# Kernel tuning notes

Hardware: AMD Instinct MI355X
Metric: run time of the kernel (lower is better)

## Reference

```python
import jax, jax.numpy as jnp
import numpy as np
from jax import lax

GAMMA = 0.99
LAM = 0.95


def setup_inputs() -> dict:
    key = jax.random.key(0)
    k1, k2, k3 = jax.random.split(key, 3)
    B, S = 4096, 4096
    rewards = jax.random.normal(k1, (B, S), dtype=jnp.float32)
    values = jax.random.normal(k2, (B, S), dtype=jnp.float32)
    next_values = jax.random.normal(k3, (B,), dtype=jnp.float32)
    return {"rewards": rewards, "values": values, "next_values": next_values}


def reference(rewards, values, next_values):
    # delta_t = r_t + gamma * V(s_{t+1}) - V(s_t); bootstrap with next_values at t = S-1
    next_v_full = jnp.concatenate([values[:, 1:], next_values[:, None]], axis=1)  # [B,S]
    deltas = rewards + GAMMA * next_v_full - values  # [B,S]

    # Reverse-time recurrence: A_t = delta_t + gamma*lam * A_{t+1}
    def step(adv, delta_t):
        adv = delta_t + (GAMMA * LAM) * adv
        return adv, adv

    deltas_rev = jnp.swapaxes(deltas, 0, 1)[::-1]  # [S,B], time-reversed
    init = jnp.zeros(rewards.shape[0], dtype=rewards.dtype)
    _, advs_rev = lax.scan(step, init, deltas_rev)  # [S,B]
    advantages = jnp.swapaxes(advs_rev[::-1], 0, 1)  # [B,S]

    returns = advantages + values
    # original detaches both outputs
    return (lax.stop_gradient(advantages), lax.stop_gradient(returns))
```

## Files before the change

kernel.cpp:

```cpp
#include <hip/hip_runtime.h>


#define GAMMA 0.99f
#define LAM   0.95f

typedef float fvec4 __attribute__((ext_vector_type(4)));

constexpr int S_LEN = 4096;
constexpr int TPB   = 256;
constexpr int NSEG  = 4;

__global__ __launch_bounds__(TPB) void gae_kernel(const float* __restrict__ rewards,
                                                  const float* __restrict__ values,
                                                  const float* __restrict__ next_values,
                                                  float* __restrict__ out, int B) {
    __shared__ float Tlds[16];

    const int b    = blockIdx.x;
    const int tid  = threadIdx.x;
    const int lane = tid & 63;
    const int w    = tid >> 6;
    const float c  = GAMMA * LAM;
    const float q4 = c * c * c * c;

    const float* vrow = values  + (size_t)b * S_LEN;
    const float* rrow = rewards + (size_t)b * S_LEN;
    const float  nv   = next_values[b];

    fvec4 v4[NSEG], r4[NSEG];
    float vn[NSEG];
#pragma unroll
    for (int s = 0; s < NSEG; ++s) {
        const int g0 = s * 1024 + 4 * tid;
        v4[s] = *(const fvec4*)(vrow + g0);
        r4[s] = *(const fvec4*)(rrow + g0);
    }
#pragma unroll
    for (int s = 0; s < NSEG; ++s) {
        const int g4 = s * 1024 + 4 * tid + 4;
        if (s == NSEG - 1 && tid == TPB - 1) vn[s] = nv;
        else                                 vn[s] = vrow[g4];
    }

    float a0[NSEG], a1[NSEG], a2[NSEG], a3[NSEG];
    float Wn[NSEG];
    float Tk = 0.f;
    float qs[6];
    {
        float qd = q4;
#pragma unroll
        for (int k = 0; k < 6; ++k) { qs[k] = qd; qd *= qd; }
    }
    const float Q256 = qs[5] * qs[5];

#pragma unroll
    for (int s = 0; s < NSEG; ++s) {
        float d3 = fmaf(GAMMA, vn[s],    r4[s].w) - v4[s].w;
        float d2 = fmaf(GAMMA, v4[s].w,  r4[s].z) - v4[s].z;
        float d1 = fmaf(GAMMA, v4[s].z,  r4[s].y) - v4[s].y;
        float d0 = fmaf(GAMMA, v4[s].y,  r4[s].x) - v4[s].x;
        float t3 = d3;
        float t2 = fmaf(c, t3, d2);
        float t1 = fmaf(c, t2, d1);
        float t0 = fmaf(c, t1, d0);
        a3[s] = t3; a2[s] = t2; a1[s] = t1; a0[s] = t0;

        float x = t0;
#pragma unroll
        for (int dlog = 0; dlog < 6; ++dlog) {
            int d = 1 << dlog;
            float other = __shfl_down(x, d);
            if (lane + d < 64) x = fmaf(qs[dlog], other, x);
        }
        Wn[s] = __shfl_down(x, 1);
        float tb = __shfl(x, 0);
        if (lane == s) Tk = tb;
    }

    if (lane < NSEG) Tlds[lane * 4 + w] = Tk;
    __syncthreads();
    float tv = (lane < 16) ? Tlds[lane] : 0.f;
    {
        float Qd = Q256;
#pragma unroll
        for (int dlog = 0; dlog < 4; ++dlog) {
            int d = 1 << dlog;
            float other = __shfl_down(tv, d);
            if (lane + d < 16) tv = fmaf(Qd, other, tv);
            Qd *= Qd;
        }
    }

    float qp = 1.f;
    {
        int e = 63 - lane;
#pragma unroll
        for (int k = 0; k < 6; ++k) if ((e >> k) & 1) qp *= qs[k];
    }

    float* adv_row = out + (size_t)b * S_LEN;
    float* ret_row = out + (size_t)B * S_LEN + (size_t)b * S_LEN;
    const float c2 = c * c, c3 = c2 * c;
#pragma unroll
    for (int s = 0; s < NSEG; ++s) {
        const int m = s * 4 + w;
        float Cm = (m == 15) ? 0.f : __shfl(tv, m + 1);
        float ct = (lane == 63) ? Cm : fmaf(qp, Cm, Wn[s]);
        float o3 = fmaf(c,  ct, a3[s]);
        float o2 = fmaf(c2, ct, a2[s]);
        float o1 = fmaf(c3, ct, a1[s]);
        float o0 = fmaf(q4, ct, a0[s]);
        const int g0 = s * 1024 + 4 * tid;
        fvec4 av; av.x = o0; av.y = o1; av.z = o2; av.w = o3;
        fvec4 rv = av + v4[s];
        __builtin_nontemporal_store(av, (fvec4*)(adv_row + g0));
        __builtin_nontemporal_store(rv, (fvec4*)(ret_row + g0));
    }
}

extern "C" void kernel_launch(void* const* d_in, const int* in_sizes, int n_in,
                              void* d_out, int out_size, void* d_ws, size_t ws_size,
                              hipStream_t stream) {
    const float* rewards     = (const float*)d_in[0];
    const float* values      = (const float*)d_in[1];
    const float* next_values = (const float*)d_in[2];
    float* out = (float*)d_out;
    const int B = in_sizes[2];
    gae_kernel<<<B, TPB, 0, stream>>>(rewards, values, next_values, out, B);
}
```

Measured before the change: 44.01 us.

## Process four rows per block with double-buffered register prefetch

Each block now handles four rows instead of one. The next row's values and rewards are loaded into a second register set while the current row is being scanned, and the LDS slot for the cross-wave carries alternates between rows. The intent is to hide global load latency behind the shuffle scan and to cut block launch overhead. In exchange the grid shrinks to B/4 blocks and register pressure roughly doubles, which can lower occupancy on a memory-bound kernel. The launch also assumes B is divisible by four.

```diff
diff --git a/kernel.cpp b/kernel.cpp
--- a/kernel.cpp
+++ b/kernel.cpp
@@ -9,42 +9,20 @@
 constexpr int S_LEN = 4096;
 constexpr int TPB   = 256;
 constexpr int NSEG  = 4;
+constexpr int ROWS  = 4;
 
 __global__ __launch_bounds__(TPB) void gae_kernel(const float* __restrict__ rewards,
                                                   const float* __restrict__ values,
                                                   const float* __restrict__ next_values,
                                                   float* __restrict__ out, int B) {
-    __shared__ float Tlds[16];
+    __shared__ float Tlds[2][16];
 
-    const int b    = blockIdx.x;
     const int tid  = threadIdx.x;
     const int lane = tid & 63;
     const int w    = tid >> 6;
     const float c  = GAMMA * LAM;
     const float q4 = c * c * c * c;
 
-    const float* vrow = values  + (size_t)b * S_LEN;
-    const float* rrow = rewards + (size_t)b * S_LEN;
-    const float  nv   = next_values[b];
-
-    fvec4 v4[NSEG], r4[NSEG];
-    float vn[NSEG];
-#pragma unroll
-    for (int s = 0; s < NSEG; ++s) {
-        const int g0 = s * 1024 + 4 * tid;
-        v4[s] = *(const fvec4*)(vrow + g0);
-        r4[s] = *(const fvec4*)(rrow + g0);
-    }
-#pragma unroll
-    for (int s = 0; s < NSEG; ++s) {
-        const int g4 = s * 1024 + 4 * tid + 4;
-        if (s == NSEG - 1 && tid == TPB - 1) vn[s] = nv;
-        else                                 vn[s] = vrow[g4];
-    }
-
-    float a0[NSEG], a1[NSEG], a2[NSEG], a3[NSEG];
-    float Wn[NSEG];
-    float Tk = 0.f;
     float qs[6];
     {
         float qd = q4;
@@ -52,70 +30,105 @@
         for (int k = 0; k < 6; ++k) { qs[k] = qd; qd *= qd; }
     }
     const float Q256 = qs[5] * qs[5];
-
-#pragma unroll
-    for (int s = 0; s < NSEG; ++s) {
-        float d3 = fmaf(GAMMA, vn[s],    r4[s].w) - v4[s].w;
-        float d2 = fmaf(GAMMA, v4[s].w,  r4[s].z) - v4[s].z;
-        float d1 = fmaf(GAMMA, v4[s].z,  r4[s].y) - v4[s].y;
-        float d0 = fmaf(GAMMA, v4[s].y,  r4[s].x) - v4[s].x;
-        float t3 = d3;
-        float t2 = fmaf(c, t3, d2);
-        float t1 = fmaf(c, t2, d1);
-        float t0 = fmaf(c, t1, d0);
-        a3[s] = t3; a2[s] = t2; a1[s] = t1; a0[s] = t0;
-
-        float x = t0;
-#pragma unroll
-        for (int dlog = 0; dlog < 6; ++dlog) {
-            int d = 1 << dlog;
-            float other = __shfl_down(x, d);
-            if (lane + d < 64) x = fmaf(qs[dlog], other, x);
-        }
-        Wn[s] = __shfl_down(x, 1);
-        float tb = __shfl(x, 0);
-        if (lane == s) Tk = tb;
-    }
-
-    if (lane < NSEG) Tlds[lane * 4 + w] = Tk;
-    __syncthreads();
-    float tv = (lane < 16) ? Tlds[lane] : 0.f;
-    {
-        float Qd = Q256;
-#pragma unroll
-        for (int dlog = 0; dlog < 4; ++dlog) {
-            int d = 1 << dlog;
-            float other = __shfl_down(tv, d);
-            if (lane + d < 16) tv = fmaf(Qd, other, tv);
-            Qd *= Qd;
-        }
-    }
-
     float qp = 1.f;
     {
         int e = 63 - lane;
 #pragma unroll
         for (int k = 0; k < 6; ++k) if ((e >> k) & 1) qp *= qs[k];
     }
+    const float c2 = c * c, c3 = c2 * c;
 
-    float* adv_row = out + (size_t)b * S_LEN;
-    float* ret_row = out + (size_t)B * S_LEN + (size_t)b * S_LEN;
-    const float c2 = c * c, c3 = c2 * c;
+    const int b0 = blockIdx.x * ROWS;
+
+    auto LOAD = [&](int b, fvec4 (&v4)[NSEG], fvec4 (&r4)[NSEG], float (&vn)[NSEG]) {
+        const float* vrow = values  + (size_t)b * S_LEN;
+        const float* rrow = rewards + (size_t)b * S_LEN;
 #pragma unroll
-    for (int s = 0; s < NSEG; ++s) {
-        const int m = s * 4 + w;
-        float Cm = (m == 15) ? 0.f : __shfl(tv, m + 1);
-        float ct = (lane == 63) ? Cm : fmaf(qp, Cm, Wn[s]);
-        float o3 = fmaf(c,  ct, a3[s]);
-        float o2 = fmaf(c2, ct, a2[s]);
-        float o1 = fmaf(c3, ct, a1[s]);
-        float o0 = fmaf(q4, ct, a0[s]);
-        const int g0 = s * 1024 + 4 * tid;
-        fvec4 av; av.x = o0; av.y = o1; av.z = o2; av.w = o3;
-        fvec4 rv = av + v4[s];
-        __builtin_nontemporal_store(av, (fvec4*)(adv_row + g0));
-        __builtin_nontemporal_store(rv, (fvec4*)(ret_row + g0));
-    }
+        for (int s = 0; s < NSEG; ++s) {
+            const int g0 = s * 1024 + 4 * tid;
+            v4[s] = *(const fvec4*)(vrow + g0);
+            r4[s] = *(const fvec4*)(rrow + g0);
+        }
+#pragma unroll
+        for (int s = 0; s < NSEG; ++s) {
+            const int g4 = s * 1024 + 4 * tid + 4;
+            if (s == NSEG - 1 && tid == TPB - 1) vn[s] = next_values[b];
+            else                                 vn[s] = vrow[g4];
+        }
+    };
+
+    auto COMPUTE = [&](int b, int par, fvec4 (&v4)[NSEG], fvec4 (&r4)[NSEG],
+                       float (&vn)[NSEG]) {
+        float a0[NSEG], a1[NSEG], a2[NSEG], a3[NSEG], Wn[NSEG];
+        float Tk = 0.f;
+#pragma unroll
+        for (int s = 0; s < NSEG; ++s) {
+            float d3 = fmaf(GAMMA, vn[s],   r4[s].w) - v4[s].w;
+            float d2 = fmaf(GAMMA, v4[s].w, r4[s].z) - v4[s].z;
+            float d1 = fmaf(GAMMA, v4[s].z, r4[s].y) - v4[s].y;
+            float d0 = fmaf(GAMMA, v4[s].y, r4[s].x) - v4[s].x;
+            float t3 = d3;
+            float t2 = fmaf(c, t3, d2);
+            float t1 = fmaf(c, t2, d1);
+            float t0 = fmaf(c, t1, d0);
+            a3[s] = t3; a2[s] = t2; a1[s] = t1; a0[s] = t0;
+
+            float x = t0;
+#pragma unroll
+            for (int dlog = 0; dlog < 6; ++dlog) {
+                int d = 1 << dlog;
+                float other = __shfl_down(x, d);
+                if (lane + d < 64) x = fmaf(qs[dlog], other, x);
+            }
+            Wn[s] = __shfl_down(x, 1);
+            float tb = __shfl(x, 0);
+            if (lane == s) Tk = tb;
+        }
+
+        if (lane < NSEG) Tlds[par][lane * 4 + w] = Tk;
+        __syncthreads();
+        float tv = (lane < 16) ? Tlds[par][lane] : 0.f;
+        {
+            float Qd = Q256;
+#pragma unroll
+            for (int dlog = 0; dlog < 4; ++dlog) {
+                int d = 1 << dlog;
+                float other = __shfl_down(tv, d);
+                if (lane + d < 16) tv = fmaf(Qd, other, tv);
+                Qd *= Qd;
+            }
+        }
+
+        float* adv_row = out + (size_t)b * S_LEN;
+        float* ret_row = out + (size_t)B * S_LEN + (size_t)b * S_LEN;
+#pragma unroll
+        for (int s = 0; s < NSEG; ++s) {
+            const int m = s * 4 + w;
+            float Cm = (m == 15) ? 0.f : __shfl(tv, m + 1);
+            float ct = (lane == 63) ? Cm : fmaf(qp, Cm, Wn[s]);
+            float o3 = fmaf(c,  ct, a3[s]);
+            float o2 = fmaf(c2, ct, a2[s]);
+            float o1 = fmaf(c3, ct, a1[s]);
+            float o0 = fmaf(q4, ct, a0[s]);
+            const int g0 = s * 1024 + 4 * tid;
+            fvec4 av; av.x = o0; av.y = o1; av.z = o2; av.w = o3;
+            fvec4 rv = av + v4[s];
+            __builtin_nontemporal_store(av, (fvec4*)(adv_row + g0));
+            __builtin_nontemporal_store(rv, (fvec4*)(ret_row + g0));
+        }
+    };
+
+    fvec4 vA[NSEG], rA[NSEG], vB[NSEG], rB[NSEG];
+    float vnA[NSEG], vnB[NSEG];
+
+    LOAD(b0 + 0, vA, rA, vnA);
+    LOAD(b0 + 1, vB, rB, vnB);
+    COMPUTE(b0 + 0, 0, vA, rA, vnA);
+    LOAD(b0 + 2, vA, rA, vnA);
+    COMPUTE(b0 + 1, 1, vB, rB, vnB);
+    LOAD(b0 + 3, vB, rB, vnB);
+    COMPUTE(b0 + 2, 0, vA, rA, vnA);
+    COMPUTE(b0 + 3, 1, vB, rB, vnB);
 }
 
 extern "C" void kernel_launch(void* const* d_in, const int* in_sizes, int n_in,
@@ -126,5 +139,5 @@
     const float* next_values = (const float*)d_in[2];
     float* out = (float*)d_out;
     const int B = in_sizes[2];
-    gae_kernel<<<B, TPB, 0, stream>>>(rewards, values, next_values, out, B);
+    gae_kernel<<<B / ROWS, TPB, 0, stream>>>(rewards, values, next_values, out, B);
 }
```

New measurement: 44.90 us. 1.02x slower.
